# Kernel tuning notes

Hardware: AMD Instinct MI355X
Metric: run time of the kernel (lower is better)

Reference implementation:

```python
import jax, jax.numpy as jnp
import numpy as np

EPS = 1e-8
N, C, R = 512, 32, 32


def _eijk():
    e = np.zeros((3, 3, 3), np.float32)
    e[0, 1, 2] = e[1, 2, 0] = e[2, 0, 1] = 1.0
    e[0, 2, 1] = e[2, 1, 0] = e[1, 0, 2] = -1.0
    return jnp.asarray(e)


def _unit(v):
    # unit_vectors: v / (|v| + EPS)
    return v / (jnp.linalg.norm(v, axis=-1, keepdims=True) + EPS)


def _y2(r):
    # real l=2 spherical harmonics (TFN convention), [N,N,5]
    x, y, z = r[..., 0], r[..., 1], r[..., 2]
    r2 = jnp.maximum(jnp.sum(r * r, axis=-1), EPS)
    c = float(2.0 * np.sqrt(3.0))
    return jnp.stack([
        x * y / r2,
        y * z / r2,
        (-x * x - y * y + 2.0 * z * z) / (c * r2),
        z * x / r2,
        (x * x - y * y) / (2.0 * r2),
    ], axis=-1)


def _forward(in0, in1, in2, rbf, rij,
             w1_f00, b1_f00, w2_f00, b2_f00,
             w1_f01, b1_f01, w2_f01, b2_f01,
             w1_f02, b1_f02, w2_f02, b2_f02,
             w1_f10, b1_f10, w2_f10, b2_f10,
             w1_f11, b1_f11, w2_f11, b2_f11):
    def rad(w1, b1, w2, b2):
        # RadialFunction: relu(b1 + rbf @ w1^T) @ w2^T + b2 -> [N,N,C]
        h = jax.nn.relu(b1 + jnp.einsum('abr,hr->abh', rbf, w1))
        return b2 + jnp.einsum('abh,ch->abc', h, w2)

    # mask self/zero-distance pairs (dij < EPS -> radial = 0), as in F_1/F_2
    mask = (jnp.linalg.norm(rij, axis=-1) >= EPS).astype(rbf.dtype)[..., None]  # [N,N,1]
    u = _unit(rij)    # [N,N,3]
    y2 = _y2(rij)     # [N,N,5]

    r00 = rad(w1_f00, b1_f00, w2_f00, b2_f00)            # scalar filter F_0
    r01 = rad(w1_f01, b1_f01, w2_f01, b2_f01) * mask     # F_1 radial, 0x1->1
    r02 = rad(w1_f02, b1_f02, w2_f02, b2_f02) * mask     # F_2 radial, 0x2->2
    r10 = rad(w1_f10, b1_f10, w2_f10, b2_f10) * mask     # F_1 radial, 1x1->0
    r11 = rad(w1_f11, b1_f11, w2_f11, b2_f11) * mask     # F_1 radial, 1x1->1

    # Filter_0_output_0 (identity CG): L x 0 -> L, aggregate over neighbors b
    o0_s = jnp.einsum('abf,bfi->afi', r00, in0)          # [N,C,1]
    o1_s = jnp.einsum('abf,bfi->afi', r00, in1)          # [N,C,3]
    o2_s = jnp.einsum('abf,bfi->afi', r00, in2)          # [N,C,5]
    o1_a = jnp.einsum('abi,abf,bf->afi', u, r01, in0[..., 0])
    o2_a = jnp.einsum('abi,abf,bf->afi', y2, r02, in0[..., 0])
    o0_b = jnp.einsum('abj,abf,bfj->af', u, r10, in1)[..., None]
    o1_c = jnp.einsum('ijk,abj,abf,bfk->afi', _eijk(), u, r11, in1)

    return (jnp.stack([o0_s, o0_b]),          # [2,N,C,1]
            jnp.stack([o1_a, o1_s, o1_c]),    # [3,N,C,3]
            jnp.stack([o2_a, o2_s]))          # [2,N,C,5]


def setup_inputs() -> dict:
    key = jax.random.key(0)
    ks = jax.random.split(key, 16)

    def xav(k, shape):
        lim = float(np.sqrt(6.0 / (shape[0] + shape[1])))
        return jax.random.uniform(k, shape, jnp.float32, -lim, lim)

    pos = jax.random.normal(ks[0], (N, 3), jnp.float32) * 3.0
    rij = pos[:, None, :] - pos[None, :, :]  # [N,N,3]; zero diagonal exercises the dij<EPS mask
    inp = {
        'in0': jax.random.normal(ks[1], (N, C, 1), jnp.float32),
        'in1': jax.random.normal(ks[2], (N, C, 3), jnp.float32),
        'in2': jax.random.normal(ks[3], (N, C, 5), jnp.float32),
        'rbf': jax.random.uniform(ks[4], (N, N, R), jnp.float32),
        'rij': rij,
    }
    for i, n in enumerate(['f00', 'f01', 'f02', 'f10', 'f11']):
        inp['w1_' + n] = xav(ks[5 + 2 * i], (R, R))
        inp['b1_' + n] = jnp.zeros((R,), jnp.float32)
        inp['w2_' + n] = xav(ks[6 + 2 * i], (C, R))
        inp['b2_' + n] = jnp.zeros((C,), jnp.float32)
    return inp


def reference(in0, in1, in2, rbf, rij,
              w1_f00, b1_f00, w2_f00, b2_f00,
              w1_f01, b1_f01, w2_f01, b2_f01,
              w1_f02, b1_f02, w2_f02, b2_f02,
              w1_f10, b1_f10, w2_f10, b2_f10,
              w1_f11, b1_f11, w2_f11, b2_f11):
    return _forward(in0, in1, in2, rbf, rij,
                    w1_f00, b1_f00, w2_f00, b2_f00,
                    w1_f01, b1_f01, w2_f01, b2_f01,
                    w1_f02, b1_f02, w2_f02, b2_f02,
                    w1_f10, b1_f10, w2_f10, b2_f10,
                    w1_f11, b1_f11, w2_f11, b2_f11)
```

## Files before the change

### kernel.cpp

```cpp
#include <hip/hip_runtime.h>
#include <math.h>

#define NN 512
#define CC 32
#define EPSF 1e-8f
#define WS 40

typedef __attribute__((ext_vector_type(8))) short bf16x8;
typedef __attribute__((ext_vector_type(4))) float f32x4;

__device__ __forceinline__ short f2bf(float f) {
    unsigned u = __float_as_uint(f);
    u += 0x7fffu + ((u >> 16) & 1u);
    return (short)(u >> 16);
}

__device__ __forceinline__ unsigned cvtpk(float lo, float hi) {
    unsigned r;
    asm("v_cvt_pk_bf16_f32 %0, %1, %2" : "=v"(r) : "v"(lo), "v"(hi));
    return r;
}

#define STAGE_F(F, W1P, W2P)                                                   \
    {                                                                          \
        wlds[(((F) * 2 + 0) * 32 + n0) * WS + k0]      = f2bf((W1P)[tid]);     \
        wlds[(((F) * 2 + 0) * 32 + n0 + 16) * WS + k0] = f2bf((W1P)[tid+512]); \
        wlds[(((F) * 2 + 1) * 32 + n0) * WS + k2]      = f2bf((W2P)[tid]);     \
        wlds[(((F) * 2 + 1) * 32 + n0 + 16) * WS + k2] = f2bf((W2P)[tid+512]); \
    }

#define MLP3S(WOFF, B1LO, B1HI, B2V, R)                                            \
    {                                                                              \
        const bf16x8 w1loM = *(const bf16x8*)&wlds[(WOFF) + ln * WS + q * 8];      \
        const bf16x8 w1hiM = *(const bf16x8*)&wlds[(WOFF) + (16 + ln) * WS + q * 8]; \
        f32x4 d0M = (B1LO);                                                        \
        f32x4 d1M = (B1HI);                                                        \
        d0M = __builtin_amdgcn_mfma_f32_16x16x32_bf16(w1loM, rbfF, d0M, 0, 0, 0);  \
        d1M = __builtin_amdgcn_mfma_f32_16x16x32_bf16(w1hiM, rbfF, d1M, 0, 0, 0);  \
        union { bf16x8 v; unsigned u[4]; } hu;                                     \
        hu.u[0] = cvtpk(fmaxf(d0M[0], 0.f), fmaxf(d0M[1], 0.f));                   \
        hu.u[1] = cvtpk(fmaxf(d0M[2], 0.f), fmaxf(d0M[3], 0.f));                   \
        hu.u[2] = cvtpk(fmaxf(d1M[0], 0.f), fmaxf(d1M[1], 0.f));                   \
        hu.u[3] = cvtpk(fmaxf(d1M[2], 0.f), fmaxf(d1M[3], 0.f));                   \
        const bf16x8 w2M = *(const bf16x8*)&wlds[(WOFF) + (32 + ch0 + ln) * WS + q * 8]; \
        f32x4 eM = { (B2V), (B2V), (B2V), (B2V) };                                 \
        R = __builtin_amdgcn_mfma_f32_16x16x32_bf16(hu.v, w2M, eM, 0, 0, 0);       \
    }

#define AGGM(RR)                                                               \
    {                                                                          \
        const int bA = b0 + q * 4 + (RR);                                      \
        const f32x4 gA = *(const f32x4*)&geomall[bA][0];                       \
        const f32x4 gB = *(const f32x4*)&geomall[bA][4];                       \
        const float i0A = in0[bA * CC + cw];                                   \
        const float* i1A = in1 + (bA * CC + cw) * 3;                           \
        const float x1A = i1A[0], y1A = i1A[1], z1A = i1A[2];                  \
        const float* i2A = in2 + (bA * CC + cw) * 5;                           \
        const float p0A = i2A[0], p1A = i2A[1], p2A = i2A[2];                  \
        const float p3A = i2A[3], p4A = i2A[4];                                \
        const float s0A = rF0[(RR)];                                           \
        a0  = fmaf(s0A, i0A, a0);                                              \
        a5  = fmaf(s0A, x1A, a5);                                              \
        a6  = fmaf(s0A, y1A, a6);                                              \
        a7  = fmaf(s0A, z1A, a7);                                              \
        a16 = fmaf(s0A, p0A, a16);                                             \
        a17 = fmaf(s0A, p1A, a17);                                             \
        a18 = fmaf(s0A, p2A, a18);                                             \
        a19 = fmaf(s0A, p3A, a19);                                             \
        a20 = fmaf(s0A, p4A, a20);                                             \
        const float t1A = rF1[(RR)] * i0A;                                     \
        a2  = fmaf(t1A, gA[0], a2);                                            \
        a3  = fmaf(t1A, gA[1], a3);                                            \
        a4  = fmaf(t1A, gA[2], a4);                                            \
        const float t2A = rF2[(RR)] * i0A;                                     \
        a11 = fmaf(t2A, gA[3], a11);                                           \
        a12 = fmaf(t2A, gB[0], a12);                                           \
        a13 = fmaf(t2A, gB[1], a13);                                           \
        a14 = fmaf(t2A, gB[2], a14);                                           \
        a15 = fmaf(t2A, gB[3], a15);                                           \
        const float dtA = fmaf(gA[2], z1A, fmaf(gA[1], y1A, gA[0] * x1A));     \
        a1  = fmaf(rF3[(RR)], dtA, a1);                                        \
        const float cxA = fmaf(gA[1], z1A, -(gA[2] * y1A));                    \
        const float cyA = fmaf(gA[2], x1A, -(gA[0] * z1A));                    \
        const float czA = fmaf(gA[0], y1A, -(gA[1] * x1A));                    \
        a8  = fmaf(rF4[(RR)], cxA, a8);                                        \
        a9  = fmaf(rF4[(RR)], cyA, a9);                                        \
        a10 = fmaf(rF4[(RR)], czA, a10);                                       \
    }

#define RED(CMP, V)                                                            \
    {                                                                          \
        float vR = (V);                                                        \
        vR += __shfl_down(vR, 32);                                             \
        vR += __shfl_down(vR, 16);                                             \
        if (lane < 16) red[(w * 21 + (CMP)) * 16 + ln] = vR;                   \
    }

__global__ __launch_bounds__(512, 2) void tfn_mfma(
    const float* __restrict__ in0,
    const float* __restrict__ in1,
    const float* __restrict__ in2,
    const float* __restrict__ rbf,
    const float* __restrict__ rij,
    const float* __restrict__ w1_0, const float* __restrict__ b1_0,
    const float* __restrict__ w2_0, const float* __restrict__ b2_0,
    const float* __restrict__ w1_1, const float* __restrict__ b1_1,
    const float* __restrict__ w2_1, const float* __restrict__ b2_1,
    const float* __restrict__ w1_2, const float* __restrict__ b1_2,
    const float* __restrict__ w2_2, const float* __restrict__ b2_2,
    const float* __restrict__ w1_3, const float* __restrict__ b1_3,
    const float* __restrict__ w2_3, const float* __restrict__ b2_3,
    const float* __restrict__ w1_4, const float* __restrict__ b1_4,
    const float* __restrict__ w2_4, const float* __restrict__ b2_4,
    float* __restrict__ out)
{
    const int a    = blockIdx.x;
    const int tid  = threadIdx.x;
    const int w    = tid >> 6;
    const int lane = tid & 63;
    const int q    = lane >> 4;
    const int ln   = lane & 15;
    const int ch0  = (w & 1) * 16;
    const int cw   = ch0 + ln;

    __shared__ short wlds[5 * 2 * 32 * WS];
    __shared__ float geomall[NN][8];

    const int n0 = tid >> 5, k0 = tid & 31;
    const int k2 = (k0 < 16) ? ((k0 >> 2) * 8 + (k0 & 3))
                             : (((k0 - 16) >> 2) * 8 + 4 + ((k0 - 16) & 3));

    STAGE_F(0, w1_0, w2_0)
    STAGE_F(1, w1_1, w2_1)
    STAGE_F(2, w1_2, w2_2)
    STAGE_F(3, w1_3, w2_3)
    STAGE_F(4, w1_4, w2_4)

    const size_t rowbase = (size_t)a * NN;
    const float Y2C = 0.28867513459481287f;

    {
        const float* rp = rij + (rowbase + tid) * 3;
        const float x = rp[0], y = rp[1], z = rp[2];
        const float d2 = x * x + y * y + z * z;
        const float d  = sqrtf(d2);
        const float m  = (d >= EPSF) ? 1.f : 0.f;
        const float inv = m / (d + EPSF);
        const float ir2 = m / fmaxf(d2, EPSF);
        f32x4 gA = { x * inv, y * inv, z * inv, x * y * ir2 };
        f32x4 gB = { y * z * ir2, (2.f * z * z - x * x - y * y) * (ir2 * Y2C),
                     z * x * ir2, (x * x - y * y) * (ir2 * 0.5f) };
        *(f32x4*)&geomall[tid][0] = gA;
        *(f32x4*)&geomall[tid][4] = gB;
    }

    const f32x4 b1lo0 = *(const f32x4*)(b1_0 + 4 * q), b1hi0 = *(const f32x4*)(b1_0 + 16 + 4 * q);
    const f32x4 b1lo1 = *(const f32x4*)(b1_1 + 4 * q), b1hi1 = *(const f32x4*)(b1_1 + 16 + 4 * q);
    const f32x4 b1lo2 = *(const f32x4*)(b1_2 + 4 * q), b1hi2 = *(const f32x4*)(b1_2 + 16 + 4 * q);
    const f32x4 b1lo3 = *(const f32x4*)(b1_3 + 4 * q), b1hi3 = *(const f32x4*)(b1_3 + 16 + 4 * q);
    const f32x4 b1lo4 = *(const f32x4*)(b1_4 + 4 * q), b1hi4 = *(const f32x4*)(b1_4 + 16 + 4 * q);
    const float b2v0 = b2_0[cw], b2v1 = b2_1[cw], b2v2 = b2_2[cw];
    const float b2v3 = b2_3[cw], b2v4 = b2_4[cw];
    __syncthreads();

    float a0 = 0.f, a1 = 0.f, a2 = 0.f, a3 = 0.f, a4 = 0.f, a5 = 0.f, a6 = 0.f;
    float a7 = 0.f, a8 = 0.f, a9 = 0.f, a10 = 0.f, a11 = 0.f, a12 = 0.f, a13 = 0.f;
    float a14 = 0.f, a15 = 0.f, a16 = 0.f, a17 = 0.f, a18 = 0.f, a19 = 0.f, a20 = 0.f;

    const int pairb = (w >> 1) * 128;

    const float* rbase = rbf + (rowbase + pairb + ln) * 32 + q * 8;
    f32x4 curA = *(const f32x4*)rbase;
    f32x4 curB = *(const f32x4*)(rbase + 4);

    #pragma unroll 1
    for (int t = 0; t < 8; ++t) {
        const int b0 = pairb + t * 16;

        union { bf16x8 v; unsigned u[4]; } ru;
        ru.u[0] = cvtpk(curA[0], curA[1]);
        ru.u[1] = cvtpk(curA[2], curA[3]);
        ru.u[2] = cvtpk(curB[0], curB[1]);
        ru.u[3] = cvtpk(curB[2], curB[3]);
        const bf16x8 rbfF = ru.v;
        if (t < 7) {
            curA = *(const f32x4*)(rbase + (t + 1) * 512);
            curB = *(const f32x4*)(rbase + (t + 1) * 512 + 4);
        }

        f32x4 rF0, rF1, rF2, rF3, rF4;
        MLP3S(0 * 64 * WS, b1lo0, b1hi0, b2v0, rF0)
        MLP3S(1 * 64 * WS, b1lo1, b1hi1, b2v1, rF1)
        MLP3S(2 * 64 * WS, b1lo2, b1hi2, b2v2, rF2)
        MLP3S(3 * 64 * WS, b1lo3, b1hi3, b2v3, rF3)
        MLP3S(4 * 64 * WS, b1lo4, b1hi4, b2v4, rF4)

        AGGM(0) AGGM(1) AGGM(2) AGGM(3)

        __builtin_amdgcn_sched_barrier(0);
    }

    __syncthreads();
    float* red = (float*)wlds;
    RED(0,  a0)  RED(1,  a1)  RED(2,  a2)  RED(3,  a3)  RED(4,  a4)
    RED(5,  a5)  RED(6,  a6)  RED(7,  a7)  RED(8,  a8)  RED(9,  a9)
    RED(10, a10) RED(11, a11) RED(12, a12) RED(13, a13) RED(14, a14)
    RED(15, a15) RED(16, a16) RED(17, a17) RED(18, a18) RED(19, a19)
    RED(20, a20)
    __syncthreads();

    const int NC = NN * CC;
    for (int e = tid; e < 21 * 32; e += 512) {
        const int cmp = e >> 5, c = e & 31;
        const int hh = c >> 4, l2 = c & 15;
        float s = 0.f;
        #pragma unroll
        for (int p = 0; p < 4; ++p)
            s += red[((p * 2 + hh) * 21 + cmp) * 16 + l2];
        int idx;
        if (cmp == 0)       idx = a * CC + c;
        else if (cmp == 1)  idx = NC + a * CC + c;
        else if (cmp < 5)   idx = 2 * NC + (a * CC + c) * 3 + (cmp - 2);
        else if (cmp < 8)   idx = 2 * NC + 3 * NC + (a * CC + c) * 3 + (cmp - 5);
        else if (cmp < 11)  idx = 2 * NC + 6 * NC + (a * CC + c) * 3 + (cmp - 8);
        else if (cmp < 16)  idx = 11 * NC + (a * CC + c) * 5 + (cmp - 11);
        else                idx = 11 * NC + 5 * NC + (a * CC + c) * 5 + (cmp - 16);
        out[idx] = s;
    }
}

extern "C" void kernel_launch(void* const* d_in, const int* in_sizes, int n_in,
                              void* d_out, int out_size, void* d_ws, size_t ws_size,
                              hipStream_t stream) {
    const float* in0 = (const float*)d_in[0];
    const float* in1 = (const float*)d_in[1];
    const float* in2 = (const float*)d_in[2];
    const float* rbf = (const float*)d_in[3];
    const float* rij = (const float*)d_in[4];

    hipLaunchKernelGGL(tfn_mfma, dim3(NN), dim3(512), 0, stream,
                       in0, in1, in2, rbf, rij,
                       (const float*)d_in[5],  (const float*)d_in[6],
                       (const float*)d_in[7],  (const float*)d_in[8],
                       (const float*)d_in[9],  (const float*)d_in[10],
                       (const float*)d_in[11], (const float*)d_in[12],
                       (const float*)d_in[13], (const float*)d_in[14],
                       (const float*)d_in[15], (const float*)d_in[16],
                       (const float*)d_in[17], (const float*)d_in[18],
                       (const float*)d_in[19], (const float*)d_in[20],
                       (const float*)d_in[21], (const float*)d_in[22],
                       (const float*)d_in[23], (const float*)d_in[24],
                       (float*)d_out);
}
```

Baseline: 40.46 us.

## Software-pipeline radial MLP one tile ahead of aggregation and pad geometry LDS rows

Restructures the neighbor loop so the MFMA radial MLP for tile t+1 is issued in the same iteration as the FMA aggregation for tile t. The rbf prefetch now runs two tiles ahead. The sched_barrier is removed so the compiler can interleave matrix and vector work. The geometry LDS row stride is widened from 8 to 12 floats, apparently to change the bank pattern. This adds 20 live registers for the next-tile filters, which risks spills or lower occupancy under the 512x2 launch bound.

```diff
diff --git a/kernel.cpp b/kernel.cpp
--- a/kernel.cpp
+++ b/kernel.cpp
@@ -5,6 +5,7 @@
 #define CC 32
 #define EPSF 1e-8f
 #define WS 40
+#define GS 12
 
 typedef __attribute__((ext_vector_type(8))) short bf16x8;
 typedef __attribute__((ext_vector_type(4))) float f32x4;
@@ -58,7 +59,7 @@
         const float* i2A = in2 + (bA * CC + cw) * 5;                           \
         const float p0A = i2A[0], p1A = i2A[1], p2A = i2A[2];                  \
         const float p3A = i2A[3], p4A = i2A[4];                                \
-        const float s0A = rF0[(RR)];                                           \
+        const float s0A = rFc0[(RR)];                                          \
         a0  = fmaf(s0A, i0A, a0);                                              \
         a5  = fmaf(s0A, x1A, a5);                                              \
         a6  = fmaf(s0A, y1A, a6);                                              \
@@ -68,24 +69,24 @@
         a18 = fmaf(s0A, p2A, a18);                                             \
         a19 = fmaf(s0A, p3A, a19);                                             \
         a20 = fmaf(s0A, p4A, a20);                                             \
-        const float t1A = rF1[(RR)] * i0A;                                     \
+        const float t1A = rFc1[(RR)] * i0A;                                    \
         a2  = fmaf(t1A, gA[0], a2);                                            \
         a3  = fmaf(t1A, gA[1], a3);                                            \
         a4  = fmaf(t1A, gA[2], a4);                                            \
-        const float t2A = rF2[(RR)] * i0A;                                     \
+        const float t2A = rFc2[(RR)] * i0A;                                    \
         a11 = fmaf(t2A, gA[3], a11);                                           \
         a12 = fmaf(t2A, gB[0], a12);                                           \
         a13 = fmaf(t2A, gB[1], a13);                                           \
         a14 = fmaf(t2A, gB[2], a14);                                           \
         a15 = fmaf(t2A, gB[3], a15);                                           \
         const float dtA = fmaf(gA[2], z1A, fmaf(gA[1], y1A, gA[0] * x1A));     \
-        a1  = fmaf(rF3[(RR)], dtA, a1);                                        \
+        a1  = fmaf(rFc3[(RR)], dtA, a1);                                       \
         const float cxA = fmaf(gA[1], z1A, -(gA[2] * y1A));                    \
         const float cyA = fmaf(gA[2], x1A, -(gA[0] * z1A));                    \
         const float czA = fmaf(gA[0], y1A, -(gA[1] * x1A));                    \
-        a8  = fmaf(rF4[(RR)], cxA, a8);                                        \
-        a9  = fmaf(rF4[(RR)], cyA, a9);                                        \
-        a10 = fmaf(rF4[(RR)], czA, a10);                                       \
+        a8  = fmaf(rFc4[(RR)], cxA, a8);                                       \
+        a9  = fmaf(rFc4[(RR)], cyA, a9);                                       \
+        a10 = fmaf(rFc4[(RR)], czA, a10);                                      \
     }
 
 #define RED(CMP, V)                                                            \
@@ -124,7 +125,7 @@
     const int cw   = ch0 + ln;
 
     __shared__ short wlds[5 * 2 * 32 * WS];
-    __shared__ float geomall[NN][8];
+    __shared__ float geomall[NN][GS];
 
     const int n0 = tid >> 5, k0 = tid & 31;
     const int k2 = (k0 < 16) ? ((k0 >> 2) * 8 + (k0 & 3))
@@ -168,36 +169,55 @@
     float a14 = 0.f, a15 = 0.f, a16 = 0.f, a17 = 0.f, a18 = 0.f, a19 = 0.f, a20 = 0.f;
 
     const int pairb = (w >> 1) * 128;
-
     const float* rbase = rbf + (rowbase + pairb + ln) * 32 + q * 8;
+
     f32x4 curA = *(const f32x4*)rbase;
     f32x4 curB = *(const f32x4*)(rbase + 4);
-
-    #pragma unroll 1
-    for (int t = 0; t < 8; ++t) {
-        const int b0 = pairb + t * 16;
-
+    f32x4 rFc0, rFc1, rFc2, rFc3, rFc4;
+    f32x4 rFn0 = {0,0,0,0}, rFn1 = {0,0,0,0}, rFn2 = {0,0,0,0};
+    f32x4 rFn3 = {0,0,0,0}, rFn4 = {0,0,0,0};
+
+    {
         union { bf16x8 v; unsigned u[4]; } ru;
         ru.u[0] = cvtpk(curA[0], curA[1]);
         ru.u[1] = cvtpk(curA[2], curA[3]);
         ru.u[2] = cvtpk(curB[0], curB[1]);
         ru.u[3] = cvtpk(curB[2], curB[3]);
         const bf16x8 rbfF = ru.v;
+        curA = *(const f32x4*)(rbase + 512);
+        curB = *(const f32x4*)(rbase + 512 + 4);
+        MLP3S(0 * 64 * WS, b1lo0, b1hi0, b2v0, rFc0)
+        MLP3S(1 * 64 * WS, b1lo1, b1hi1, b2v1, rFc1)
+        MLP3S(2 * 64 * WS, b1lo2, b1hi2, b2v2, rFc2)
+        MLP3S(3 * 64 * WS, b1lo3, b1hi3, b2v3, rFc3)
+        MLP3S(4 * 64 * WS, b1lo4, b1hi4, b2v4, rFc4)
+    }
+
+    #pragma unroll 1
+    for (int t = 0; t < 8; ++t) {
+        const int b0 = pairb + t * 16;
+
         if (t < 7) {
-            curA = *(const f32x4*)(rbase + (t + 1) * 512);
-            curB = *(const f32x4*)(rbase + (t + 1) * 512 + 4);
+            union { bf16x8 v; unsigned u[4]; } ru;
+            ru.u[0] = cvtpk(curA[0], curA[1]);
+            ru.u[1] = cvtpk(curA[2], curA[3]);
+            ru.u[2] = cvtpk(curB[0], curB[1]);
+            ru.u[3] = cvtpk(curB[2], curB[3]);
+            const bf16x8 rbfF = ru.v;
+            if (t < 6) {
+                curA = *(const f32x4*)(rbase + (t + 2) * 512);
+                curB = *(const f32x4*)(rbase + (t + 2) * 512 + 4);
+            }
+            MLP3S(0 * 64 * WS, b1lo0, b1hi0, b2v0, rFn0)
+            MLP3S(1 * 64 * WS, b1lo1, b1hi1, b2v1, rFn1)
+            MLP3S(2 * 64 * WS, b1lo2, b1hi2, b2v2, rFn2)
+            MLP3S(3 * 64 * WS, b1lo3, b1hi3, b2v3, rFn3)
+            MLP3S(4 * 64 * WS, b1lo4, b1hi4, b2v4, rFn4)
         }
 
-        f32x4 rF0, rF1, rF2, rF3, rF4;
-        MLP3S(0 * 64 * WS, b1lo0, b1hi0, b2v0, rF0)
-        MLP3S(1 * 64 * WS, b1lo1, b1hi1, b2v1, rF1)
-        MLP3S(2 * 64 * WS, b1lo2, b1hi2, b2v2, rF2)
-        MLP3S(3 * 64 * WS, b1lo3, b1hi3, b2v3, rF3)
-        MLP3S(4 * 64 * WS, b1lo4, b1hi4, b2v4, rF4)
-
         AGGM(0) AGGM(1) AGGM(2) AGGM(3)
 
-        __builtin_amdgcn_sched_barrier(0);
+        rFc0 = rFn0; rFc1 = rFn1; rFc2 = rFn2; rFc3 = rFn3; rFc4 = rFn4;
     }
 
     __syncthreads();
```

Result: slower. 67.09 us (+65.8%).
